# Performance work log

Hardware: AMD Instinct MI355X
Metric: run time of the kernel (lower is better)

The kernel has to match this reference:

```python
import jax, jax.numpy as jnp
import numpy as np
from jax import lax

NUM_CHANNELS = 3
NUM_HEADS = 8
PATCH = 16  # projection_dim = 3 * 16 * 16 = 768
EPS = 1e-5


def setup_inputs() -> dict:
    key = jax.random.key(0)
    ks = jax.random.split(key, 16)
    B, N, D, Hdim = 4, 1024, 768, 3072
    H = NUM_HEADS

    def init(k, shape, fan_in):
        bound = 1.0 / np.sqrt(fan_in)
        return jax.random.uniform(k, shape, jnp.float32, -bound, bound)

    return {
        "x": jax.random.normal(ks[0], (B, N, D), jnp.float32),
        # 3x3 conv QKV projections over per-patch [3,16,16] images (no bias, qkv_bias=False)
        "qconv_w": init(ks[1], (NUM_CHANNELS, NUM_CHANNELS, 3, 3), NUM_CHANNELS * 9),
        "kconv_w": init(ks[2], (NUM_CHANNELS, NUM_CHANNELS, 3, 3), NUM_CHANNELS * 9),
        "vconv_w": init(ks[3], (NUM_CHANNELS, NUM_CHANNELS, 3, 3), NUM_CHANNELS * 9),
        # 1x1 conv mixing heads of the attention map + BatchNorm2d(heads)
        "reatten_w": init(ks[4], (H, H), H),
        "reatten_b": init(ks[5], (H,), H),
        "bn_g": jnp.ones((H,), jnp.float32),
        "bn_b": jnp.zeros((H,), jnp.float32),
        # output projection (Linear dim->dim)
        "proj_w": init(ks[6], (D, D), D),
        "proj_b": init(ks[7], (D,), D),
        # LayerNorm over (num_patches, projection_dim) jointly
        "ln_g": jnp.ones((N, D), jnp.float32),
        "ln_b": jnp.zeros((N, D), jnp.float32),
        # FeedForward
        "ff_w1": init(ks[8], (Hdim, D), D),
        "ff_b1": init(ks[9], (Hdim,), D),
        "ff_w2": init(ks[10], (D, Hdim), Hdim),
        "ff_b2": init(ks[11], (D,), Hdim),
    }


def _conv3x3(x, w):
    # x: [BN, C, p, p], w: [C, C, 3, 3], stride 1, SAME padding
    return lax.conv_general_dilated(x, w, (1, 1), "SAME",
                                    dimension_numbers=("NCHW", "OIHW", "NCHW"))


def _layernorm_2d(x, g, b):
    # LayerNorm over last two axes (N, D) jointly, biased variance, eps=1e-5
    mu = jnp.mean(x, axis=(-2, -1), keepdims=True)
    var = jnp.mean(jnp.square(x - mu), axis=(-2, -1), keepdims=True)
    return (x - mu) * lax.rsqrt(var + EPS) * g + b


def _encoder_fwd(x, qconv_w, kconv_w, vconv_w, reatten_w, reatten_b,
                 bn_g, bn_b, proj_w, proj_b, ln_g, ln_b,
                 ff_w1, ff_b1, ff_w2, ff_b2):
    B, N, D = x.shape
    H = NUM_HEADS
    hd = D // H
    scale = hd ** -0.5

    # --- ReAttention ---
    xi = x.reshape(B * N, NUM_CHANNELS, PATCH, PATCH)

    def qkv(w):
        y = _conv3x3(xi, w).reshape(B, N, H, hd)
        return y.transpose(0, 2, 1, 3)  # [B, H, N, hd]

    q, k, v = qkv(qconv_w), qkv(kconv_w), qkv(vconv_w)

    attn = jax.nn.softmax(jnp.einsum("bhnd,bhmd->bhnm", q, k) * scale, axis=-1)

    # learned cross-head 1x1 conv + BatchNorm2d (training-mode batch stats)
    attn = jnp.einsum("gh,bhnm->bgnm", reatten_w, attn) + reatten_b[None, :, None, None]
    mu = jnp.mean(attn, axis=(0, 2, 3), keepdims=True)
    var = jnp.mean(jnp.square(attn - mu), axis=(0, 2, 3), keepdims=True)
    attn = (attn - mu) * lax.rsqrt(var + EPS)
    attn = attn * bn_g[None, :, None, None] + bn_b[None, :, None, None]

    out = jnp.einsum("bhnm,bhmd->bhnd", attn, v)
    out = out.transpose(0, 2, 1, 3).reshape(B, N, D)
    out = out @ proj_w.T + proj_b

    # --- residual + LN ---
    x1 = _layernorm_2d(x + out, ln_g, ln_b)

    # --- FeedForward (exact GELU) + residual + LN ---
    h = jax.nn.gelu(x1 @ ff_w1.T + ff_b1, approximate=False)
    ff = h @ ff_w2.T + ff_b2
    return _layernorm_2d(x1 + ff, ln_g, ln_b)


def reference(x, qconv_w, kconv_w, vconv_w, reatten_w, reatten_b,
              bn_g, bn_b, proj_w, proj_b, ln_g, ln_b,
              ff_w1, ff_b1, ff_w2, ff_b2):
    return _encoder_fwd(x, qconv_w, kconv_w, vconv_w, reatten_w, reatten_b,
                        bn_g, bn_b, proj_w, proj_b, ln_g, ln_b,
                        ff_w1, ff_b1, ff_w2, ff_b2)
```

## Files before the change

### kernel.cpp

```cpp
#include <hip/hip_runtime.h>
#include <math.h>


typedef unsigned short u16;
typedef unsigned int u32;
typedef __bf16 bf16x8 __attribute__((ext_vector_type(8)));
typedef float f32x4 __attribute__((ext_vector_type(4)));

#define EPSV 1e-5f
#define SL2E 0.14724444620253177f
#define EXPC -11.541560327111707f

__device__ __forceinline__ u16 f2bf(float f) {
  union { float f; u32 u; } v; v.f = f;
  u32 u = v.u + 0x7fffu + ((v.u >> 16) & 1u);
  return (u16)(u >> 16);
}
__device__ __forceinline__ float bf2f(u16 h) {
  union { u32 u; float f; } v; v.u = ((u32)h) << 16; return v.f;
}
__device__ __forceinline__ f32x4 mfma16(bf16x8 a, bf16x8 b, f32x4 c) {
  return __builtin_amdgcn_mfma_f32_16x16x32_bf16(a, b, c, 0, 0, 0);
}
__device__ __forceinline__ void gload16(const void* gp, void* lp) {
  __builtin_amdgcn_global_load_lds(
      (const __attribute__((address_space(1))) u32*)gp,
      (__attribute__((address_space(3))) u32*)lp, 16, 0, 0);
}

struct KS { int off[3]; int hl[3]; };
__device__ __forceinline__ KS ks_init(int t) {
  KS ks;
  int lane = t & 63;
  int lh = lane >> 4, l15 = lane & 15;
  #pragma unroll
  for (int j = 0; j < 3; ++j) {
    int G = j * 512 + t;
    int hl = (G >= 768) ? 1 : 0;
    int C = (G - hl * 768) >> 6;
    int chunk = C / 6, r = C - 6 * chunk;
    int kk = r >> 1, c1 = r & 1;
    int m = chunk * 32 + ((l15 >> 2) << 3) + (c1 << 2) + (l15 & 3);
    ks.off[j] = m * 96 + kk * 32 + lh * 8;
    ks.hl[j] = hl;
  }
  return ks;
}
__device__ __forceinline__ void ks_stage(const u16* __restrict__ khi,
    const u16* __restrict__ klo, size_t rowel, const KS& ks, u16* Kb, int t) {
  int w = t >> 6;
  #pragma unroll
  for (int j = 0; j < 3; ++j) {
    const u16* src = (ks.hl[j] ? klo : khi) + rowel + ks.off[j];
    gload16(src, Kb + (size_t)(j * 512 + w * 64) * 8);
  }
}

__device__ __forceinline__ void qload(const u16* __restrict__ qhi,
    const u16* __restrict__ qlo, size_t qoff, bf16x8* qh, bf16x8* ql) {
  #pragma unroll
  for (int kk = 0; kk < 3; ++kk) {
    qh[kk] = *(const bf16x8*)(qhi + qoff + kk * 32);
    ql[kk] = *(const bf16x8*)(qlo + qoff + kk * 32);
  }
}

__device__ __forceinline__ void score18(const u16* Kb, int mh, int lane,
    const bf16x8* qh, const bf16x8* ql, f32x4& C0, f32x4& C1) {
  C0 = (f32x4){0.f, 0.f, 0.f, 0.f};
  C1 = (f32x4){0.f, 0.f, 0.f, 0.f};
  #pragma unroll
  for (int kk = 0; kk < 3; ++kk) {
    const u16* base = Kb + (mh * 6 + kk * 2) * 512 + lane * 8;
    bf16x8 kh0 = *(const bf16x8*)(base);
    bf16x8 kh1 = *(const bf16x8*)(base + 512);
    bf16x8 kl0 = *(const bf16x8*)(base + 6144);
    bf16x8 kl1 = *(const bf16x8*)(base + 6656);
    C0 = mfma16(kh0, qh[kk], C0);
    C0 = mfma16(kl0, qh[kk], C0);
    C0 = mfma16(kh0, ql[kk], C0);
    C1 = mfma16(kh1, qh[kk], C1);
    C1 = mfma16(kl1, qh[kk], C1);
    C1 = mfma16(kh1, ql[kk], C1);
  }
}

__global__ __launch_bounds__(256) void k_f2b(const float* __restrict__ s,
                                             u16* __restrict__ d, int n) {
  int i = blockIdx.x * 256 + threadIdx.x;
  int stride = gridDim.x * 256;
  for (; i < n; i += stride) d[i] = f2bf(s[i]);
}

__global__ __launch_bounds__(256) void k_conv(const float* __restrict__ x,
    const float* __restrict__ wq, const float* __restrict__ wk, const float* __restrict__ wv,
    u16* __restrict__ qhi, u16* __restrict__ qlo,
    u16* __restrict__ khi, u16* __restrict__ klo,
    float* __restrict__ vb)
{
  __shared__ float patch[768], swq[81], swk[81], swv[81];
  int bid = blockIdx.x;
  int b = bid >> 10, n = bid & 1023;
  int t = threadIdx.x;
  const float* xr = x + (size_t)bid * 768;
  patch[t] = xr[t]; patch[t + 256] = xr[t + 256]; patch[t + 512] = xr[t + 512];
  if (t < 81) { swq[t] = wq[t]; swk[t] = wk[t]; swv[t] = wv[t]; }
  __syncthreads();
  #pragma unroll
  for (int r = 0; r < 3; ++r) {
    int f = t + 256 * r;
    int o = f >> 8, rem = f & 255, pp = rem >> 4, qq = rem & 15;
    float aq = 0.f, ak = 0.f, av = 0.f;
    #pragma unroll
    for (int i = 0; i < 3; ++i)
      #pragma unroll
      for (int dp = 0; dp < 3; ++dp) {
        int ip = pp + dp - 1;
        if (ip < 0 || ip > 15) continue;
        #pragma unroll
        for (int dq = 0; dq < 3; ++dq) {
          int iq = qq + dq - 1;
          if (iq < 0 || iq > 15) continue;
          float pv = patch[i * 256 + ip * 16 + iq];
          int wi = ((o * 3 + i) * 3 + dp) * 3 + dq;
          aq += swq[wi] * pv; ak += swk[wi] * pv; av += swv[wi] * pv;
        }
      }
    int h = f / 96, d = f - h * 96;
    size_t oi = ((size_t)(b * 8 + h) * 1024 + n) * 96 + d;
    float aqs = aq * SL2E;
    u16 qh_ = f2bf(aqs); qhi[oi] = qh_; qlo[oi] = f2bf(aqs - bf2f(qh_));
    u16 kh_ = f2bf(ak);  khi[oi] = kh_; klo[oi] = f2bf(ak - bf2f(kh_));
    vb[oi] = av;
  }
}

__global__ __launch_bounds__(256) void k_vtr(const float* __restrict__ vb,
                                             u16* __restrict__ vtr)
{
  __shared__ u16 lds[12288];
  int bid = blockIdx.x;
  int bh = bid >> 3, n0 = (bid & 7) * 128;
  int t = threadIdx.x;
  int n = t >> 1, dh = (t & 1) * 48;
  const float* src = vb + ((size_t)bh * 1024 + n0 + n) * 96 + dh;
  #pragma unroll
  for (int j4 = 0; j4 < 12; ++j4) {
    float4 v = *(const float4*)(src + j4 * 4);
    int d = dh + j4 * 4;
    lds[(d + 0) * 128 + n] = f2bf(v.x);
    lds[(d + 1) * 128 + n] = f2bf(v.y);
    lds[(d + 2) * 128 + n] = f2bf(v.z);
    lds[(d + 3) * 128 + n] = f2bf(v.w);
  }
  __syncthreads();
  #pragma unroll
  for (int j = 0; j < 48; ++j) {
    int flat = t + 256 * j;
    int d = flat >> 7, n2 = flat & 127;
    vtr[((size_t)bh * 96 + d) * 1024 + n0 + n2] = lds[flat];
  }
}

__global__ __launch_bounds__(512, 2) void k_score(
    const u16* __restrict__ qhi, const u16* __restrict__ qlo,
    const u16* __restrict__ khi, const u16* __restrict__ klo,
    float* __restrict__ zp, u16* __restrict__ pt)
{
  __shared__ u16 Kst[2][12288];
  int p = blockIdx.x;
  int s = p >> 3;
  int c = (p & 7) * 4 + (s >> 4);
  int ng = s & 15;
  int b = c >> 3, mg = c & 7;
  int t = threadIdx.x, lane = t & 63, w = t >> 6;
  int l15 = lane & 15, lhi = lane >> 4;
  int nsub = w >> 1, mh = w & 1;
  int n0 = ng * 64 + nsub * 16;
  int nt = ng * 4 + nsub;
  int m0base = mg * 128;
  KS ks = ks_init(t);
  bf16x8 qh[3], ql[3], qh2[3], ql2[3];
  size_t bh0 = (size_t)(b * 8) * 1024;
  ks_stage(khi, klo, (bh0 + m0base) * 96, ks, Kst[0], t);
  qload(qhi, qlo, (bh0 + n0 + l15) * 96 + lhi * 8, qh, ql);
  __syncthreads();
  #pragma unroll 1
  for (int h = 0; h < 8; ++h) {
    float z = 0.f;
    #pragma unroll
    for (int mt = 0; mt < 2; ++mt) {
      int u = h * 2 + mt;
      if (u < 15) {
        int un = u + 1, hn = un >> 1, mtn = un & 1;
        size_t bhn = (size_t)(b * 8 + hn) * 1024;
        ks_stage(khi, klo, (bhn + m0base + mtn * 64) * 96, ks, Kst[(u + 1) & 1], t);
        if (mtn == 0)
          qload(qhi, qlo, (bhn + n0 + l15) * 96 + lhi * 8, qh2, ql2);
      }
      f32x4 C0, C1;
      score18(Kst[u & 1], mh, lane, qh, ql, C0, C1);
      union { u16 us[8]; uint4 q4; } pk;
      #pragma unroll
      for (int r = 0; r < 4; ++r) {
        float e0 = exp2f(C0[r] + EXPC);
        float e1 = exp2f(C1[r] + EXPC);
        z += e0 + e1;
        pk.us[r]     = f2bf(e0);
        pk.us[4 + r] = f2bf(e1);
      }
      int mc = mg * 4 + mt * 2 + mh;
      *(uint4*)&pt[((((size_t)(b * 8 + h) * 32 + mc) * 64 + nt) * 64 + lane) * 8] = pk.q4;
      if (u < 15 && mt == 1) {
        #pragma unroll
        for (int kk = 0; kk < 3; ++kk) { qh[kk] = qh2[kk]; ql[kk] = ql2[kk]; }
      }
      __syncthreads();
    }
    z += __shfl_xor(z, 16);
    z += __shfl_xor(z, 32);
    if (lane < 16)
      zp[((size_t)((b * 8 + h) * 16 + mg * 2 + mh)) * 1024 + n0 + lane] = z;
  }
}

__global__ __launch_bounds__(256) void k_zmerge(const float* __restrict__ zp,
                                                float* __restrict__ invZ)
{
  int idx = blockIdx.x * 256 + threadIdx.x;
  int bh = idx >> 10, n = idx & 1023;
  float z = 0.f;
  #pragma unroll
  for (int s = 0; s < 16; ++s) z += zp[((size_t)(bh * 16 + s)) * 1024 + n];
  invZ[idx] = 1.f / z;
}

__global__ __launch_bounds__(256) void k_mix(
    u16* __restrict__ pt, const float* __restrict__ invZ,
    const float* __restrict__ rw, float* __restrict__ pstat)
{
  __shared__ float red[4][16];
  int t = threadIdx.x;
  int gid = blockIdx.x * 256 + t;
  int half = gid & 1;
  int lane = (gid >> 1) & 63;
  int nt = (gid >> 7) & 63;
  int mc = (gid >> 13) & 31;
  int b  = gid >> 18;
  int n = nt * 16 + (lane & 15);
  float iz[8];
  #pragma unroll
  for (int h = 0; h < 8; ++h) iz[h] = invZ[(b * 8 + h) * 1024 + n];
  float out[8][4];
  #pragma unroll
  for (int g = 0; g < 8; ++g) {
    float wsum = 0.f;
    #pragma unroll
    for (int h = 0; h < 8; ++h) wsum += rw[g * 8 + h];
    float cg = -wsum * (1.f / 1024.f);
    #pragma unroll
    for (int e = 0; e < 4; ++e) out[g][e] = cg;
  }
  size_t base = ((((size_t)(b * 8) * 32 + mc) * 64 + nt) * 64 + lane) * 8 + half * 4;
  #pragma unroll
  for (int h = 0; h < 8; ++h) {
    uint2 gr = *(const uint2*)(pt + base + (size_t)h * 1048576);
    float izh = iz[h];
    union { u32 u; float f; } c0, c1, c2, c3;
    c0.u = gr.x << 16;
    c1.u = gr.x & 0xffff0000u;
    c2.u = gr.y << 16;
    c3.u = gr.y & 0xffff0000u;
    float q0 = c0.f * izh, q1 = c1.f * izh, q2 = c2.f * izh, q3 = c3.f * izh;
    #pragma unroll
    for (int g = 0; g < 8; ++g) {
      float wgh = rw[g * 8 + h];
      out[g][0] += wgh * q0;
      out[g][1] += wgh * q1;
      out[g][2] += wgh * q2;
      out[g][3] += wgh * q3;
    }
  }
  float sc[8], scc[8];
  #pragma unroll
  for (int g = 0; g < 8; ++g) {
    float o0 = out[g][0], o1 = out[g][1], o2 = out[g][2], o3 = out[g][3];
    sc[g] = (o0 + o1) + (o2 + o3);
    scc[g] = (o0 * o0 + o1 * o1) + (o2 * o2 + o3 * o3);
    uint2 pk;
    pk.x = (u32)f2bf(o0) | ((u32)f2bf(o1) << 16);
    pk.y = (u32)f2bf(o2) | ((u32)f2bf(o3) << 16);
    *(uint2*)(pt + base + (size_t)g * 1048576) = pk;
  }
  int wv = t >> 6, lane2 = t & 63;
  #pragma unroll
  for (int off = 32; off > 0; off >>= 1)
    #pragma unroll
    for (int g = 0; g < 8; ++g) {
      sc[g] += __shfl_down(sc[g], off);
      scc[g] += __shfl_down(scc[g], off);
    }
  if (lane2 == 0) {
    #pragma unroll
    for (int g = 0; g < 8; ++g) {
      red[wv][g] = sc[g];
      red[wv][8 + g] = scc[g];
    }
  }
  __syncthreads();
  if (t < 16)
    pstat[(size_t)blockIdx.x * 16 + t] =
        red[0][t] + red[1][t] + red[2][t] + red[3][t];
}

__global__ __launch_bounds__(256, 4) void k_pv(
    const u16* __restrict__ pt, const u16* __restrict__ vtr,
    float* __restrict__ U0, float* __restrict__ U1)
{
  int p = blockIdx.x;
  int t = threadIdx.x, lane = t & 63, w = t >> 6;
  int l15 = lane & 15, lhi = lane >> 4;
  int xcd = p & 7;
  int i = p >> 3;
  int pair = xcd * 4 + (i >> 5);
  int rest = i & 31;
  int ntq = rest >> 1, mhf = rest & 1;
  int b = pair >> 3, g = pair & 7;
  int nt = ntq * 4 + w;
  f32x4 acc[6];
  #pragma unroll
  for (int ds = 0; ds < 6; ++ds) acc[ds] = (f32x4){0.f, 0.f, 0.f, 0.f};
  size_t pbase = ((((size_t)(b * 8 + g) * 32) * 64 + nt) * 64 + lane);
  size_t vbase = (size_t)(b * 8 + g) * 96;
  #pragma unroll 2
  for (int mc = mhf * 16; mc < mhf * 16 + 16; ++mc) {
    bf16x8 pf = *(const bf16x8*)(pt + (pbase + (size_t)mc * 4096) * 8);
    int mof = mc * 32 + lhi * 8;
    #pragma unroll
    for (int ds = 0; ds < 6; ++ds) {
      bf16x8 vf = *(const bf16x8*)(vtr + (vbase + ds * 16 + l15) * 1024 + mof);
      acc[ds] = mfma16(pf, vf, acc[ds]);
    }
  }
  float* Uq = mhf ? U1 : U0;
  #pragma unroll
  for (int ds = 0; ds < 6; ++ds)
    #pragma unroll
    for (int r = 0; r < 4; ++r) {
      int n = nt * 16 + lhi * 4 + r;
      Uq[((size_t)(b * 1024 + n)) * 768 + g * 96 + ds * 16 + l15] = acc[ds][r];
    }
}

__global__ __launch_bounds__(384) void k_vcs(const float* __restrict__ vb,
                                             float* __restrict__ vcs)
{
  __shared__ float part[4][96];
  int bh = blockIdx.x, t = threadIdx.x;
  int c = t % 96, g4 = t / 96;
  float a = 0.f;
  const float* vp = vb + (size_t)bh * 98304 + (size_t)g4 * 24576 + c;
  for (int m = 0; m < 256; ++m) a += vp[m * 96];
  part[g4][c] = a;
  __syncthreads();
  if (t < 96) vcs[bh * 96 + t] = part[0][t] + part[1][t] + part[2][t] + part[3][t];
}

__global__ __launch_bounds__(256) void k_statred(const float* __restrict__ pstat,
                                                 float* __restrict__ stats)
{
  __shared__ float part[16][17];
  int t = threadIdx.x;
  int j = t >> 4, s = t & 15;
  float a = 0.f;
  for (int k2 = 0; k2 < 256; ++k2)
    a += pstat[(size_t)(s + 16 * k2) * 16 + j];
  part[j][s] = a;
  __syncthreads();
  if (t < 16) {
    float v = 0.f;
    #pragma unroll
    for (int s2 = 0; s2 < 16; ++s2) v += part[t][s2];
    stats[t] = v;
  }
}

__global__ __launch_bounds__(256) void k_bnfin(const float* __restrict__ U0,
    const float* __restrict__ U1, const float* __restrict__ vcs,
    const float* __restrict__ stats, const float* __restrict__ bng,
    const float* __restrict__ bnb, u16* __restrict__ ubb)
{
  size_t idx = (size_t)blockIdx.x * 256 + threadIdx.x;
  int col = (int)(idx % 768); int i = (int)(idx / 768); int b = i >> 10;
  int g = col / 96, d = col - g * 96;
  const float cnt = 4194304.f;
  float mc = stats[g] / cnt;
  float var = stats[8 + g] / cnt - mc * mc;
  float sg = bng[g] * rsqrtf(var + EPSV);
  float tg = bnb[g] - sg * mc;
  ubb[idx] = f2bf(sg * (U0[idx] + U1[idx]) + tg * vcs[(b * 8 + g) * 96 + d]);
}

template<int GELU_, int RES_, int STATS_, int BF16OUT>
__global__ __launch_bounds__(256) void k_gemm(
    const u16* __restrict__ A, const u16* __restrict__ W,
    const float* __restrict__ bias, const float* __restrict__ res,
    float* __restrict__ out, u16* __restrict__ outb,
    int K, int Nc, float* __restrict__ stats)
{
  __shared__ u16 As[8192], Bs[8192];
  __shared__ float red[8];
  int t = threadIdx.x, lane = t & 63, wv = t >> 6;
  int l15 = lane & 15, lhi = lane >> 4;
  int i0 = blockIdx.y * 128, j0 = blockIdx.x * 128;
  int wr = wv >> 1, wc = wv & 1;
  f32x4 acc[4][4];
  #pragma unroll
  for (int mi = 0; mi < 4; ++mi)
    #pragma unroll
    for (int ni = 0; ni < 4; ++ni) acc[mi][ni] = (f32x4){0.f, 0.f, 0.f, 0.f};
  int rA = lane >> 3;
  int colel = 8 * ((lane & 7) ^ rA);
  for (int k0 = 0; k0 < K; k0 += 64) {
    if (k0) __syncthreads();
    #pragma unroll
    for (int i = 0; i < 4; ++i) {
      int cA = wv * 4 + i;
      int r = cA * 8 + rA;
      gload16(A + (size_t)(i0 + r) * K + k0 + colel, &As[cA * 512]);
      gload16(W + (size_t)(j0 + r) * K + k0 + colel, &Bs[cA * 512]);
    }
    __syncthreads();
    #pragma unroll
    for (int ks = 0; ks < 2; ++ks) {
      bf16x8 af[4], bf[4];
      #pragma unroll
      for (int mi = 0; mi < 4; ++mi) {
        int r2 = wr * 64 + mi * 16 + l15;
        af[mi] = *(const bf16x8*)&As[r2 * 64 + ((ks * 32 + lhi * 8) ^ (8 * (r2 & 7)))];
      }
      #pragma unroll
      for (int ni = 0; ni < 4; ++ni) {
        int r3 = wc * 64 + ni * 16 + l15;
        bf[ni] = *(const bf16x8*)&Bs[r3 * 64 + ((ks * 32 + lhi * 8) ^ (8 * (r3 & 7)))];
      }
      #pragma unroll
      for (int mi = 0; mi < 4; ++mi)
        #pragma unroll
        for (int ni = 0; ni < 4; ++ni)
          acc[mi][ni] = mfma16(af[mi], bf[ni], acc[mi][ni]);
    }
  }
  float ls = 0.f, lss = 0.f;
  #pragma unroll
  for (int mi = 0; mi < 4; ++mi) {
    #pragma unroll
    for (int ni = 0; ni < 4; ++ni) {
      int col = j0 + wc * 64 + ni * 16 + l15;
      float bv = bias[col];
      #pragma unroll
      for (int r = 0; r < 4; ++r) {
        int row = i0 + wr * 64 + mi * 16 + lhi * 4 + r;
        float val = acc[mi][ni][r] + bv;
        if (RES_) val += res[(size_t)row * Nc + col];
        if (GELU_) val = 0.5f * val * (1.f + erff(val * 0.70710678118654752f));
        if (BF16OUT) outb[(size_t)row * Nc + col] = f2bf(val);
        else out[(size_t)row * Nc + col] = val;
        if (STATS_) { ls += val; lss += val * val; }
      }
    }
  }
  if (STATS_) {
    #pragma unroll
    for (int off = 32; off > 0; off >>= 1) {
      ls += __shfl_down(ls, off); lss += __shfl_down(lss, off);
    }
    if (lane == 0) { red[wv * 2] = ls; red[wv * 2 + 1] = lss; }
    __syncthreads();
    if (t == 0) {
      int b = i0 >> 10;
      atomicAdd(&stats[b * 2],     red[0] + red[2] + red[4] + red[6]);
      atomicAdd(&stats[b * 2 + 1], red[1] + red[3] + red[5] + red[7]);
    }
  }
}

template<int BF16OUT>
__global__ __launch_bounds__(256) void k_ln(const float* __restrict__ y,
    const float* __restrict__ stats, const float* __restrict__ g,
    const float* __restrict__ bta, float* __restrict__ outp, u16* __restrict__ outb)
{
  size_t idx = (size_t)blockIdx.x * 256 + threadIdx.x;
  int i = (int)(idx / 768), col = (int)(idx % 768);
  int b = i >> 10, n = i & 1023;
  const float cnt = 786432.f;
  float mu = stats[b * 2] / cnt;
  float var = stats[b * 2 + 1] / cnt - mu * mu;
  float r = rsqrtf(var + EPSV);
  size_t gi = (size_t)n * 768 + col;
  float v = (y[idx] - mu) * r * g[gi] + bta[gi];
  outp[idx] = v;
  if (BF16OUT) outb[idx] = f2bf(v);
}

extern "C" void kernel_launch(void* const* d_in, const int* in_sizes, int n_in,
                              void* d_out, int out_size, void* d_ws, size_t ws_size,
                              hipStream_t stream)
{
  const float* x   = (const float*)d_in[0];
  const float* qw  = (const float*)d_in[1];
  const float* kw  = (const float*)d_in[2];
  const float* vw  = (const float*)d_in[3];
  const float* rw  = (const float*)d_in[4];
  const float* bng = (const float*)d_in[6];
  const float* bnb = (const float*)d_in[7];
  const float* pw  = (const float*)d_in[8];
  const float* pb  = (const float*)d_in[9];
  const float* lng = (const float*)d_in[10];
  const float* lnb = (const float*)d_in[11];
  const float* fw1 = (const float*)d_in[12];
  const float* fb1 = (const float*)d_in[13];
  const float* fw2 = (const float*)d_in[14];
  const float* fb2 = (const float*)d_in[15];
  float* out = (float*)d_out;

  u16* pt   = (u16*)d_ws;
  float* vb = (float*)pt;
  u16* hb   = pt;
  float* y2 = (float*)pt + 12582912;
  float* fsm = (float*)(pt + 33554432);
  float* stats = fsm;
  float* pstat = fsm + 64;
  float* vcs   = fsm + 65600;
  float* zp    = fsm + 68672;
  float* invZ  = fsm + 592960;
  u16* qhi  = (u16*)(fsm + 625728);
  u16* qlo  = qhi + 3145728;
  u16* khi  = qlo + 3145728;
  u16* klo  = khi + 3145728;
  u16* vtrb = klo + 3145728;
  u16* pwb  = vtrb + 3145728;
  u16* fw1b = pwb + 589824;
  u16* fw2b = fw1b + 2359296;
  float* U0 = (float*)qhi;
  float* U1 = (float*)khi;
  float* x1 = (float*)khi;
  float* y1 = U0;
  u16* ubb  = vtrb;
  u16* x1b  = vtrb;

  hipMemsetAsync(stats, 0, 64 * sizeof(float), stream);
  k_f2b<<<1024, 256, 0, stream>>>(pw, pwb, 589824);
  k_f2b<<<2048, 256, 0, stream>>>(fw1, fw1b, 2359296);
  k_f2b<<<2048, 256, 0, stream>>>(fw2, fw2b, 2359296);

  k_conv<<<4096, 256, 0, stream>>>(x, qw, kw, vw, qhi, qlo, khi, klo, vb);
  k_vtr<<<256, 256, 0, stream>>>(vb, vtrb);
  k_vcs<<<32, 384, 0, stream>>>(vb, vcs);
  k_score<<<512, 512, 0, stream>>>(qhi, qlo, khi, klo, zp, pt);
  k_zmerge<<<128, 256, 0, stream>>>(zp, invZ);
  k_mix<<<4096, 256, 0, stream>>>(pt, invZ, rw, pstat);
  k_pv<<<1024, 256, 0, stream>>>(pt, vtrb, U0, U1);
  k_statred<<<1, 256, 0, stream>>>(pstat, stats);
  k_bnfin<<<12288, 256, 0, stream>>>(U0, U1, vcs, stats, bng, bnb, ubb);

  k_gemm<0,1,1,0><<<dim3(6, 32), 256, 0, stream>>>(ubb, pwb, pb, x, y1, nullptr, 768, 768, stats + 16);
  k_ln<1><<<12288, 256, 0, stream>>>(y1, stats + 16, lng, lnb, x1, x1b);
  k_gemm<1,0,0,1><<<dim3(24, 32), 256, 0, stream>>>(x1b, fw1b, fb1, nullptr, nullptr, hb, 768, 3072, nullptr);
  k_gemm<0,1,1,0><<<dim3(6, 32), 256, 0, stream>>>(hb, fw2b, fb2, x1, y2, nullptr, 3072, 768, stats + 24);
  k_ln<0><<<12288, 256, 0, stream>>>(y2, stats + 24, lng, lnb, out, nullptr);
}
```

Baseline: 336.8 us.

## Split-K the FFN down-projection GEMM and parallelize the BN stat reduction

The second FFN GEMM (K=3072, only 192 blocks) is split into three K-slices, giving 576 blocks that write fp32 partials. A new finisher kernel sums the partials, adds bias and residual, and accumulates the LayerNorm statistics. The single-block BN statistics reduction becomes a two-stage reduction over 64 blocks. This trades extra partial-buffer traffic and one more launch for better occupancy on the underfilled GPU.

```diff
diff --git a/kernel.cpp b/kernel.cpp
--- a/kernel.cpp
+++ b/kernel.cpp
@@ -366,15 +366,36 @@
   if (t < 96) vcs[bh * 96 + t] = part[0][t] + part[1][t] + part[2][t] + part[3][t];
 }
 
-__global__ __launch_bounds__(256) void k_statred(const float* __restrict__ pstat,
-                                                 float* __restrict__ stats)
+__global__ __launch_bounds__(256) void k_statred1(const float* __restrict__ pstat,
+                                                  float* __restrict__ pred)
+{
+  __shared__ float part[16][17];
+  int bb = blockIdx.x, t = threadIdx.x;
+  int j = t >> 4, s = t & 15;
+  float a = 0.f;
+  #pragma unroll
+  for (int k2 = 0; k2 < 4; ++k2)
+    a += pstat[(size_t)(bb * 64 + s + 16 * k2) * 16 + j];
+  part[j][s] = a;
+  __syncthreads();
+  if (t < 16) {
+    float v = 0.f;
+    #pragma unroll
+    for (int s2 = 0; s2 < 16; ++s2) v += part[t][s2];
+    pred[bb * 16 + t] = v;
+  }
+}
+
+__global__ __launch_bounds__(256) void k_statred2(const float* __restrict__ pred,
+                                                  float* __restrict__ stats)
 {
   __shared__ float part[16][17];
   int t = threadIdx.x;
   int j = t >> 4, s = t & 15;
   float a = 0.f;
-  for (int k2 = 0; k2 < 256; ++k2)
-    a += pstat[(size_t)(s + 16 * k2) * 16 + j];
+  #pragma unroll
+  for (int k2 = 0; k2 < 4; ++k2)
+    a += pred[(size_t)(s + 16 * k2) * 16 + j];
   part[j][s] = a;
   __syncthreads();
   if (t < 16) {
@@ -482,6 +503,93 @@
       atomicAdd(&stats[b * 2],     red[0] + red[2] + red[4] + red[6]);
       atomicAdd(&stats[b * 2 + 1], red[1] + red[3] + red[5] + red[7]);
     }
+  }
+}
+
+__global__ __launch_bounds__(256) void k_gemm_part(
+    const u16* __restrict__ A, const u16* __restrict__ W,
+    float* __restrict__ P, int K, int KSfull, int Nc)
+{
+  __shared__ u16 As[8192], Bs[8192];
+  int t = threadIdx.x, lane = t & 63, wv = t >> 6;
+  int l15 = lane & 15, lhi = lane >> 4;
+  int i0 = blockIdx.y * 128, j0 = blockIdx.x * 128;
+  int kz = blockIdx.z;
+  int kbase = kz * K;
+  float* out = P + (size_t)kz * 4096 * Nc;
+  int wr = wv >> 1, wc = wv & 1;
+  f32x4 acc[4][4];
+  #pragma unroll
+  for (int mi = 0; mi < 4; ++mi)
+    #pragma unroll
+    for (int ni = 0; ni < 4; ++ni) acc[mi][ni] = (f32x4){0.f, 0.f, 0.f, 0.f};
+  int rA = lane >> 3;
+  int colel = 8 * ((lane & 7) ^ rA);
+  for (int k0 = 0; k0 < K; k0 += 64) {
+    if (k0) __syncthreads();
+    #pragma unroll
+    for (int i = 0; i < 4; ++i) {
+      int cA = wv * 4 + i;
+      int r = cA * 8 + rA;
+      gload16(A + (size_t)(i0 + r) * KSfull + kbase + k0 + colel, &As[cA * 512]);
+      gload16(W + (size_t)(j0 + r) * KSfull + kbase + k0 + colel, &Bs[cA * 512]);
+    }
+    __syncthreads();
+    #pragma unroll
+    for (int ks = 0; ks < 2; ++ks) {
+      bf16x8 af[4], bf[4];
+      #pragma unroll
+      for (int mi = 0; mi < 4; ++mi) {
+        int r2 = wr * 64 + mi * 16 + l15;
+        af[mi] = *(const bf16x8*)&As[r2 * 64 + ((ks * 32 + lhi * 8) ^ (8 * (r2 & 7)))];
+      }
+      #pragma unroll
+      for (int ni = 0; ni < 4; ++ni) {
+        int r3 = wc * 64 + ni * 16 + l15;
+        bf[ni] = *(const bf16x8*)&Bs[r3 * 64 + ((ks * 32 + lhi * 8) ^ (8 * (r3 & 7)))];
+      }
+      #pragma unroll
+      for (int mi = 0; mi < 4; ++mi)
+        #pragma unroll
+        for (int ni = 0; ni < 4; ++ni)
+          acc[mi][ni] = mfma16(af[mi], bf[ni], acc[mi][ni]);
+    }
+  }
+  #pragma unroll
+  for (int mi = 0; mi < 4; ++mi)
+    #pragma unroll
+    for (int ni = 0; ni < 4; ++ni) {
+      int col = j0 + wc * 64 + ni * 16 + l15;
+      #pragma unroll
+      for (int r = 0; r < 4; ++r) {
+        int row = i0 + wr * 64 + mi * 16 + lhi * 4 + r;
+        out[(size_t)row * Nc + col] = acc[mi][ni][r];
+      }
+    }
+}
+
+__global__ __launch_bounds__(256) void k_fin2(const float* __restrict__ P,
+    const float* __restrict__ bias, const float* __restrict__ res,
+    float* __restrict__ y, float* __restrict__ stats)
+{
+  __shared__ float red[8];
+  size_t idx = (size_t)blockIdx.x * 256 + threadIdx.x;
+  int col = (int)(idx % 768);
+  int b = (int)(idx / 786432);
+  float v = (P[idx] + P[idx + 3145728]) + (P[idx + 6291456] + bias[col]) +
+            res[idx];
+  y[idx] = v;
+  float ls = v, lss = v * v;
+  int t = threadIdx.x, lane = t & 63, wv = t >> 6;
+  #pragma unroll
+  for (int off = 32; off > 0; off >>= 1) {
+    ls += __shfl_down(ls, off); lss += __shfl_down(lss, off);
+  }
+  if (lane == 0) { red[wv * 2] = ls; red[wv * 2 + 1] = lss; }
+  __syncthreads();
+  if (t == 0) {
+    atomicAdd(&stats[b * 2],     red[0] + red[2] + red[4] + red[6]);
+    atomicAdd(&stats[b * 2 + 1], red[1] + red[3] + red[5] + red[7]);
   }
 }
 
@@ -527,7 +635,7 @@
   u16* pt   = (u16*)d_ws;
   float* vb = (float*)pt;
   u16* hb   = pt;
-  float* y2 = (float*)pt + 12582912;
+  float* pfin = (float*)(pt + 12582912);
   float* fsm = (float*)(pt + 33554432);
   float* stats = fsm;
   float* pstat = fsm + 64;
@@ -546,6 +654,8 @@
   float* U1 = (float*)khi;
   float* x1 = (float*)khi;
   float* y1 = U0;
+  float* y2 = U0;
+  float* pred = zp;
   u16* ubb  = vtrb;
   u16* x1b  = vtrb;
 
@@ -561,12 +671,14 @@
   k_zmerge<<<128, 256, 0, stream>>>(zp, invZ);
   k_mix<<<4096, 256, 0, stream>>>(pt, invZ, rw, pstat);
   k_pv<<<1024, 256, 0, stream>>>(pt, vtrb, U0, U1);
-  k_statred<<<1, 256, 0, stream>>>(pstat, stats);
+  k_statred1<<<64, 256, 0, stream>>>(pstat, pred);
+  k_statred2<<<1, 256, 0, stream>>>(pred, stats);
   k_bnfin<<<12288, 256, 0, stream>>>(U0, U1, vcs, stats, bng, bnb, ubb);
 
   k_gemm<0,1,1,0><<<dim3(6, 32), 256, 0, stream>>>(ubb, pwb, pb, x, y1, nullptr, 768, 768, stats + 16);
   k_ln<1><<<12288, 256, 0, stream>>>(y1, stats + 16, lng, lnb, x1, x1b);
   k_gemm<1,0,0,1><<<dim3(24, 32), 256, 0, stream>>>(x1b, fw1b, fb1, nullptr, nullptr, hb, 768, 3072, nullptr);
-  k_gemm<0,1,1,0><<<dim3(6, 32), 256, 0, stream>>>(hb, fw2b, fb2, x1, y2, nullptr, 3072, 768, stats + 24);
+  k_gemm_part<<<dim3(6, 32, 3), 256, 0, stream>>>(hb, fw2b, pfin, 1024, 3072, 768);
+  k_fin2<<<12288, 256, 0, stream>>>(pfin, fb2, x1, y2, stats + 24);
   k_ln<0><<<12288, 256, 0, stream>>>(y2, stats + 24, lng, lnb, out, nullptr);
 }
```

Measured after the change: 603.2 us. 1.79x slower.
